# Optimization experiments

Measured on AMD Instinct MI355X. Metric: run time of the kernel, lower is better.

## Reference

```python
import jax, jax.numpy as jnp
import numpy as np

NS, NV = 48, 10
N_NODES, N_EDGES = 10000, 100000
N_EDGE_FEAT = 3 * NS  # 144
W_SS, W_VS, W_SV, W_VV = NS * NS, NV * NS, NS * NV, NV * NV
W_NUMEL = W_SS + W_VS + W_SV + W_VV  # 3364 = FullyConnectedTensorProduct.weight_numel
IN_DIM = NS + 3 * NV  # 78
EPS = 1e-5


def setup_inputs() -> dict:
    key = jax.random.key(0)
    ks = jax.random.split(key, 8)
    return {
        "node_attr": jax.random.normal(ks[0], (N_NODES, IN_DIM), jnp.float32),
        "edge_attr": jax.random.normal(ks[1], (N_EDGES, N_EDGE_FEAT), jnp.float32),
        "edge_sh": jax.random.normal(ks[2], (N_EDGES, 4), jnp.float32),
        "fc1_w": jax.random.normal(ks[3], (N_EDGE_FEAT, N_EDGE_FEAT), jnp.float32) / np.sqrt(N_EDGE_FEAT).astype(np.float32),
        "fc1_b": jnp.zeros((N_EDGE_FEAT,), jnp.float32),
        "fc2_w": jax.random.normal(ks[4], (N_EDGE_FEAT, W_NUMEL), jnp.float32) / np.sqrt(N_EDGE_FEAT).astype(np.float32),
        "fc2_b": jnp.zeros((W_NUMEL,), jnp.float32),
        "bn_weight": jnp.ones((NS + NV,), jnp.float32),
        "bn_bias": jnp.zeros((NS,), jnp.float32),
        "edge_index": jax.random.randint(ks[5], (2, N_EDGES), 0, N_NODES),
    }


def reference(node_attr, edge_attr, edge_sh, fc1_w, fc1_b, fc2_w, fc2_b, bn_weight, bn_bias, edge_index):
    edge_src, edge_dst = edge_index[0], edge_index[1]
    # --- gather node feats per edge, split into irreps ---
    x = node_attr[edge_dst]                      # [E, 78]
    xs = x[:, :NS]                               # [E, 48]  scalars (0e)
    xv = x[:, NS:].reshape(-1, NV, 3)            # [E, 10, 3] vectors (1o)
    s0 = edge_sh[:, 0]                           # [E]     sh 0e
    s1 = edge_sh[:, 1:4]                         # [E, 3]  sh 1o

    # --- per-edge TP weights from edge MLP ---
    w = jax.nn.relu(edge_attr @ fc1_w + fc1_b) @ fc2_w + fc2_b  # [E, 3364]
    w_ss = w[:, :W_SS].reshape(-1, NS, NS)
    w_vs = w[:, W_SS:W_SS + W_VS].reshape(-1, NV, NS)
    w_sv = w[:, W_SS + W_VS:W_SS + W_VS + W_SV].reshape(-1, NS, NV)
    w_vv = w[:, W_SS + W_VS + W_SV:].reshape(-1, NV, NV)

    # path normalization: 1/sqrt(mul_in * n_paths_into_output_irrep)
    a_ss = 1.0 / np.sqrt(NS * 2.0)
    a_vs = 1.0 / np.sqrt(NV * 2.0)
    a_sv = 1.0 / np.sqrt(NS * 2.0)
    a_vv = 1.0 / np.sqrt(NV * 2.0)

    # --- Clebsch-Gordan tensor product (fully connected, per-edge weights) ---
    # 0e (x) 0e -> 0e
    out_s = a_ss * jnp.einsum('ei,eio->eo', xs, w_ss) * s0[:, None]
    # 1o (x) 1o -> 0e  (CG = delta/sqrt(3))
    dot = jnp.einsum('eic,ec->ei', xv, s1) / np.sqrt(3.0)
    out_s = out_s + a_vs * jnp.einsum('ei,eio->eo', dot, w_vs)
    # 0e (x) 1o -> 1o
    out_v = a_sv * jnp.einsum('ei,eio->eo', xs, w_sv)[:, :, None] * s1[:, None, :]
    # 1o (x) 0e -> 1o
    out_v = out_v + a_vv * jnp.einsum('eic,eio->eoc', xv, w_vv) * s0[:, None, None]

    tp = jnp.concatenate([out_s, out_v.reshape(-1, 3 * NV)], axis=1)  # [E, 78]

    # --- scatter-mean to nodes ---
    sums = jax.ops.segment_sum(tp, edge_src, num_segments=N_NODES)
    cnt = jax.ops.segment_sum(jnp.ones((tp.shape[0],), tp.dtype), edge_src, num_segments=N_NODES)
    out = sums / jnp.maximum(cnt, 1.0)[:, None]

    # --- residual (in_dim == out_dim -> pad is a no-op) ---
    out = out + node_attr

    # --- equivariant batch norm (e3nn-style, batch statistics) ---
    os = out[:, :NS]
    ov = out[:, NS:].reshape(-1, NV, 3)
    mu = os.mean(0)
    var = os.var(0)
    os = (os - mu) / jnp.sqrt(var + EPS) * bn_weight[:NS] + bn_bias
    fn = (ov ** 2).sum(-1).mean(0) / 3.0  # component-normalized mean squared norm per channel
    ov = ov / jnp.sqrt(fn + EPS)[None, :, None] * bn_weight[NS:][None, :, None]
    return jnp.concatenate([os, ov.reshape(-1, 3 * NV)], axis=1)
```

## Files before the change

kernel.cpp:

```cpp
#include <hip/hip_runtime.h>
#include <hip/hip_bf16.h>

#define NS   48
#define NV   10
#define NEF  144
#define WN   3364
#define IND  78
#define NE   100000
#define NN   10000
#define EPS  1e-5f
#define HP   144
#define EB   128

#define A_SS 0.10206207261596575f
#define A_VS 0.22360679774997896f
#define A_SV 0.10206207261596575f
#define A_VV 0.22360679774997896f
#define RS3  0.5773502691896258f

typedef __attribute__((ext_vector_type(8)))  short    short8;
typedef __attribute__((ext_vector_type(16))) float    f32x16;
typedef __attribute__((ext_vector_type(4)))  int      int4v;
typedef __attribute__((ext_vector_type(4)))  float    float4v;
typedef __attribute__((ext_vector_type(2)))  __fp16   fp16x2;
typedef __attribute__((ext_vector_type(8)))  _Float16 half8;

#define MFMAH(a,b,c) __builtin_amdgcn_mfma_f32_32x32x16_f16((a),(b),(c),0,0,0)

#define TP_F    0
#define CNT_F   7800160
#define OFFS_F  7810160
#define CUR_F   7820164
#define EL_F    7830164
#define PART_F  7930164
#define RAW_F   8320164
#define WSBF_F  8320324

#define OFF_W1  0
#define OFF_B1  23040
#define OFF_B2  468480
#define OFF_B3  561664
#define N_PREP  608256

__device__ __forceinline__ short toh(float v) {
    return __builtin_bit_cast(short, (_Float16)v);
}
__device__ __forceinline__ float fromh(short s) {
    return (float)__builtin_bit_cast(_Float16, s);
}
__device__ __forceinline__ unsigned pkh2(float a, float b) {
    fp16x2 h = __builtin_amdgcn_cvt_pkrtz(a, b);
    return __builtin_bit_cast(unsigned, h);
}
__device__ __forceinline__ float waveReduceSum(float v) {
    #pragma unroll
    for (int o = 32; o > 0; o >>= 1) v += __shfl_down(v, o, 64);
    return v;
}
__device__ __forceinline__ void gl_lds16(const short* g, short* l) {
    __builtin_amdgcn_global_load_lds(
        (const __attribute__((address_space(1))) unsigned int*)g,
        (__attribute__((address_space(3))) unsigned int*)l, 16, 0, 0);
}

__device__ __forceinline__ float prep_fetch(int idx, const float* __restrict__ fc1_w,
                                            const float* __restrict__ fc2_w,
                                            const float* __restrict__ b2)
{
    float v = 0.f;
    if (idx < OFF_B1) {
        int r = idx;
        int tile = r / 4608, rem = r % 4608;
        int ks = rem / 512, l = (rem % 512) / 8, j = rem % 8;
        int n = tile * 32 + (l & 31);
        int k = ks * 16 + ((l >> 5) << 3) + j;
        v = (n < 144) ? fc1_w[k * 144 + n] : 0.f;
    } else if (idx < OFF_B2) {
        int r = idx - OFF_B1;
        if (r < 442368) {
            int i = r / 9216, rem = r % 9216;
            int tile = rem / 4608; rem %= 4608;
            int ks = rem / 512, l = (rem % 512) / 8, j = rem % 8;
            int n = tile * 32 + (l & 31);
            int k = ks * 16 + ((l >> 5) << 3) + j;
            if (n < 48)      v = fc2_w[(size_t)k * WN + i * 48 + n];
            else if (n < 58) v = fc2_w[(size_t)k * WN + 2784 + i * 10 + (n - 48)];
        } else {
            int rb = r - 442368;
            int tile = rb / 1536, rem = rb % 1536;
            int ks = rem / 512, l = (rem % 512) / 8, j = rem % 8;
            int n = tile * 32 + (l & 31);
            int k = ks * 16 + ((l >> 5) << 3) + j;
            if (n < 48)      v = b2[k * 48 + n];
            else if (n < 58) v = b2[2784 + k * 10 + (n - 48)];
        }
    } else if (idx < OFF_B3) {
        int r = idx - OFF_B2;
        if (r < 92160) {
            int i = r / 9216, rem = r % 9216;
            int tile = rem / 4608; rem %= 4608;
            int ks = rem / 512, l = (rem % 512) / 8, j = rem % 8;
            int n = tile * 32 + (l & 31);
            int k = ks * 16 + ((l >> 5) << 3) + j;
            if (n < 48) v = fc2_w[(size_t)k * WN + 2304 + i * 48 + n];
        } else {
            int rb = r - 92160;
            int tile = rb / 512, rem = rb % 512;
            int l = rem / 8, j = rem % 8;
            int n = tile * 32 + (l & 31);
            int k = ((l >> 5) << 3) + j;
            if (k < 10 && n < 48) v = b2[2304 + k * 48 + n];
        }
    } else {
        int r = idx - OFF_B3;
        if (r < 46080) {
            int i = r / 4608, rem = r % 4608;
            int ks = rem / 512, l = (rem % 512) / 8, j = rem % 8;
            int n = l & 31;
            int k = ks * 16 + ((l >> 5) << 3) + j;
            if (n < 10) v = fc2_w[(size_t)k * WN + 3264 + i * 10 + n];
        } else {
            int rb = r - 46080;
            int l = rb / 8, j = rb % 8;
            int n = l & 31;
            int k = ((l >> 5) << 3) + j;
            if (k < 10 && n < 10) v = b2[3264 + k * 10 + n];
        }
    }
    return v;
}

__global__ void prep_weights(const float* __restrict__ fc1_w,
                             const float* __restrict__ fc2_w,
                             const float* __restrict__ b2,
                             short* __restrict__ wsbf)
{
    int tid = blockIdx.x * 256 + threadIdx.x;
    if (tid >= N_PREP / 8) return;
    int base = tid * 8;
    short8 outv;
    #pragma unroll
    for (int j = 0; j < 8; ++j)
        outv[j] = toh(prep_fetch(base + j, fc1_w, fc2_w, b2));
    *reinterpret_cast<short8*>(wsbf + base) = outv;
}

__global__ void hist_kernel(const int* __restrict__ eidx, int* __restrict__ cntI)
{
    int e = blockIdx.x * 256 + threadIdx.x;
    if (e < NE) atomicAdd(&cntI[eidx[e]], 1);
}

__global__ __launch_bounds__(1024) void scan_kernel(const int* __restrict__ cntI,
                                                    int* __restrict__ offs,
                                                    int* __restrict__ cursor)
{
    __shared__ int part[1024];
    int t = threadIdx.x;
    int base = t * 10;
    int local[10];
    int s = 0;
    #pragma unroll
    for (int q = 0; q < 10; ++q) {
        int i = base + q;
        int v = (i < NN) ? cntI[i] : 0;
        local[q] = s; s += v;
    }
    part[t] = s;
    __syncthreads();
    for (int o = 1; o < 1024; o <<= 1) {
        int v = (t >= o) ? part[t - o] : 0;
        __syncthreads();
        part[t] += v;
        __syncthreads();
    }
    int prev = (t == 0) ? 0 : part[t - 1];
    #pragma unroll
    for (int q = 0; q < 10; ++q) {
        int i = base + q;
        if (i < NN) { int val = prev + local[q]; offs[i] = val; cursor[i] = val; }
    }
    if (t == 1023) offs[NN] = part[1023];
}

__global__ void scatter_kernel(const int* __restrict__ eidx,
                               int* __restrict__ cursor, int* __restrict__ elist)
{
    int e = blockIdx.x * 256 + threadIdx.x;
    if (e < NE) {
        int pos = atomicAdd(&cursor[eidx[e]], 1);
        elist[pos] = e;
    }
}

__global__ __launch_bounds__(256, 2) void fused_main(
    const float* __restrict__ node_attr, const float* __restrict__ edge_attr,
    const float* __restrict__ edge_sh,   const float* __restrict__ b1,
    const int*   __restrict__ eidx,      const short* __restrict__ wsbf,
    float* __restrict__ tp)
{
    __shared__ short ubuf[18432];
    __shared__ short xfT[96 * EB];
    __shared__ float pbuf[EB][10];
    __shared__ float s0s[EB];
    __shared__ float s1s[EB][3];

    const int t    = threadIdx.x;
    const int e0   = blockIdx.x * EB;
    const int lane = t & 63, wave = t >> 6;
    const int n32  = lane & 31, kh = lane >> 5;
    const int eL   = 32 * wave + n32;
    const int eLc  = min(e0 + eL, NE - 1);

    const short* W1L = wsbf + OFF_W1 + lane * 8;
    const short* B1L = wsbf + OFF_B1 + lane * 8;
    const short* B2L = wsbf + OFF_B2 + lane * 8;
    const short* B3L = wsbf + OFF_B3 + lane * 8;

    auto stageB = [&](const short* src, short* dst, int nfrag) {
        for (int f = wave; f < nfrag; f += 4)
            gl_lds16(src + f * 512 + lane * 8, dst + f * 512);
    };

    for (int idx = t; idx < 8 * EB; idx += 256) xfT[88 * EB + idx] = 0;

    if (t < EB) {
        int ee = e0 + t;
        if (ee < NE) {
            float4v sh = *reinterpret_cast<const float4v*>(edge_sh + (size_t)ee * 4);
            s0s[t] = sh.x; s1s[t][0] = sh.y; s1s[t][1] = sh.z; s1s[t][2] = sh.w;
        } else {
            s0s[t] = 0.f; s1s[t][0] = s1s[t][1] = s1s[t][2] = 0.f;
        }
    }

    {
        const int eg  = t & (EB - 1);
        const int jb  = t >> 7;
        const int egc = min(e0 + eg, NE - 1);
        const int dst = eidx[NE + egc];
        const float* na = node_attr + (size_t)dst * IND;
        for (int j = jb; j < IND; j += 2) {
            int slot = (j < NS) ? j : 58 + ((j - NS) % 3) * 10 + (j - NS) / 3;
            xfT[slot * EB + eg] = toh(na[j]);
        }
    }

    half8 afc[9];
    {
        const float* ea = edge_attr + (size_t)eLc * NEF + kh * 8;
        #pragma unroll
        for (int ks = 0; ks < 9; ++ks) {
            float4v lo = *reinterpret_cast<const float4v*>(ea + ks * 16);
            float4v hi = *reinterpret_cast<const float4v*>(ea + ks * 16 + 4);
            int4v v = { (int)pkh2(lo.x, lo.y), (int)pkh2(lo.z, lo.w),
                        (int)pkh2(hi.x, hi.y), (int)pkh2(hi.z, hi.w) };
            afc[ks] = __builtin_bit_cast(half8, v);
        }
    }
    __syncthreads();

    #pragma unroll
    for (int it = 0; it < 5; ++it) {
        int e = t & (EB - 1);
        int i = (t >> 7) + 2 * it;
        float d = fromh(xfT[(58 + i) * EB + e]) * s1s[e][0]
                + fromh(xfT[(68 + i) * EB + e]) * s1s[e][1]
                + fromh(xfT[(78 + i) * EB + e]) * s1s[e][2];
        xfT[(48 + i) * EB + e] = toh(d * RS3);
    }

    for (int pass = 0; pass < 3; ++pass) {
        int ntA = 2 * pass, ntB = 2 * pass + 1;
        bool hasB = (pass < 2);
        f32x16 accA = 0, accB = 0;
        #pragma unroll
        for (int ks = 0; ks < 9; ++ks) {
            half8 bA = *(const half8*)(W1L + (ntA * 9 + ks) * 512);
            accA = MFMAH(afc[ks], bA, accA);
            if (hasB) {
                half8 bB = *(const half8*)(W1L + (ntB * 9 + ks) * 512);
                accB = MFMAH(afc[ks], bB, accB);
            }
        }
        int colA = ntA * 32 + n32, colB = ntB * 32 + n32;
        float b1A = (colA < NEF) ? b1[colA] : 0.f;
        float b1B = (hasB && colB < NEF) ? b1[colB] : 0.f;
        #pragma unroll
        for (int r = 0; r < 16; ++r) {
            int row = (r & 3) + 8 * (r >> 2) + 4 * kh;
            int e = 32 * wave + row;
            if (colA < NEF) ubuf[e * HP + colA] = toh(fmaxf(accA[r] + b1A, 0.f));
            if (hasB)       ubuf[e * HP + colB] = toh(fmaxf(accB[r] + b1B, 0.f));
        }
    }

    half8 hh[9];
    #pragma unroll
    for (int ks = 0; ks < 9; ++ks)
        hh[ks] = *(const half8*)(ubuf + eL * HP + ks * 16 + kh * 8);
    __syncthreads();

    short* stg0 = ubuf;
    short* stg1 = ubuf + 9216;

    stageB(wsbf + OFF_B1, stg0, 18);
    __syncthreads();

    auto splat8 = [&](int slot) -> half8 {
        _Float16 xh = __builtin_bit_cast(_Float16, xfT[slot * EB + eL]);
        half8 r = { xh, xh, xh, xh, xh, xh, xh, xh };
        return r;
    };

    f32x16 acc1a = 0, acc1b = 0, acc2a = 0, acc2b = 0;
    {
        #pragma unroll 1
        for (int i = 0; i < 48; ++i) {
            short* cur = (i & 1) ? stg1 : stg0;
            short* nxt = (i & 1) ? stg0 : stg1;
            if (i < 47) stageB(wsbf + OFF_B1 + (i + 1) * 9216, nxt, 18);
            else        stageB(wsbf + OFF_B2, nxt, 18);
            half8 x8 = splat8(i);
            #pragma unroll
            for (int ks = 0; ks < 9; ++ks) {
                half8 a  = hh[ks] * x8;
                half8 b0 = *(const half8*)(cur + ks * 512 + lane * 8);
                half8 b1f= *(const half8*)(cur + 4608 + ks * 512 + lane * 8);
                acc1a = MFMAH(a, b0, acc1a);
                acc1b = MFMAH(a, b1f, acc1b);
            }
            __syncthreads();
        }
        #pragma unroll
        for (int ks = 0; ks < 3; ++ks) {
            short8 a;
            #pragma unroll
            for (int j = 0; j < 8; ++j)
                a[j] = xfT[(ks * 16 + kh * 8 + j) * EB + eL];
            half8 ah = __builtin_bit_cast(half8, a);
            half8 b0 = *(const half8*)(B1L + 442368 + ks * 512);
            half8 b1f= *(const half8*)(B1L + 442368 + 1536 + ks * 512);
            acc1a = MFMAH(ah, b0, acc1a);
            acc1b = MFMAH(ah, b1f, acc1b);
        }
    }
    {
        #pragma unroll 1
        for (int i = 0; i < 10; ++i) {
            short* cur = (i & 1) ? stg1 : stg0;
            short* nxt = (i & 1) ? stg0 : stg1;
            if (i < 9) stageB(wsbf + OFF_B2 + (i + 1) * 9216, nxt, 18);
            else       stageB(wsbf + OFF_B3, nxt, 9);
            half8 x8 = splat8(48 + i);
            #pragma unroll
            for (int ks = 0; ks < 9; ++ks) {
                half8 a  = hh[ks] * x8;
                half8 b0 = *(const half8*)(cur + ks * 512 + lane * 8);
                half8 b1f= *(const half8*)(cur + 4608 + ks * 512 + lane * 8);
                acc2a = MFMAH(a, b0, acc2a);
                acc2b = MFMAH(a, b1f, acc2b);
            }
            __syncthreads();
        }
        {
            short8 a;
            #pragma unroll
            for (int j = 0; j < 8; ++j)
                a[j] = xfT[(48 + kh * 8 + j) * EB + eL];
            half8 ah = __builtin_bit_cast(half8, a);
            half8 b0 = *(const half8*)(B2L + 92160);
            half8 b1f= *(const half8*)(B2L + 92160 + 512);
            acc2a = MFMAH(ah, b0, acc2a);
            acc2b = MFMAH(ah, b1f, acc2b);
        }
    }
    #pragma unroll
    for (int r = 0; r < 16; ++r) {
        int row = (r & 3) + 8 * (r >> 2) + 4 * kh;
        int e = 32 * wave + row;
        int ge = e0 + e;
        if (ge < NE) {
            float s0e = s0s[e];
            float* rowp = tp + (size_t)ge * IND;
            rowp[n32] = A_SS * s0e * acc1a[r] + A_VS * acc2a[r];
            int col = 32 + n32;
            if (col < 48) {
                rowp[col] = A_SS * s0e * acc1b[r] + A_VS * acc2b[r];
            } else if (col < 58) {
                pbuf[e][col - 48] = A_SV * acc1b[r];
            }
        }
    }
    {
        f32x16 acc30 = 0, acc31 = 0, acc32 = 0;
        #pragma unroll 1
        for (int i = 0; i < 10; ++i) {
            short* cur = (i & 1) ? stg1 : stg0;
            short* nxt = (i & 1) ? stg0 : stg1;
            if (i < 9) stageB(wsbf + OFF_B3 + (i + 1) * 4608, nxt, 9);
            half8 x0 = splat8(58 + i), x1 = splat8(68 + i), x2 = splat8(78 + i);
            #pragma unroll
            for (int ks = 0; ks < 9; ++ks) {
                half8 b0 = *(const half8*)(cur + ks * 512 + lane * 8);
                acc30 = MFMAH(hh[ks] * x0, b0, acc30);
                acc31 = MFMAH(hh[ks] * x1, b0, acc31);
                acc32 = MFMAH(hh[ks] * x2, b0, acc32);
            }
            __syncthreads();
        }
        {
            half8 bb = *(const half8*)(B3L + 46080);
            short8 a;
            #pragma unroll
            for (int j = 0; j < 8; ++j) a[j] = xfT[(58 + kh * 8 + j) * EB + eL];
            acc30 = MFMAH(__builtin_bit_cast(half8, a), bb, acc30);
            #pragma unroll
            for (int j = 0; j < 8; ++j) a[j] = xfT[(68 + kh * 8 + j) * EB + eL];
            acc31 = MFMAH(__builtin_bit_cast(half8, a), bb, acc31);
            #pragma unroll
            for (int j = 0; j < 8; ++j) a[j] = xfT[(78 + kh * 8 + j) * EB + eL];
            acc32 = MFMAH(__builtin_bit_cast(half8, a), bb, acc32);
        }
        if (n32 < 10) {
            #pragma unroll
            for (int r = 0; r < 16; ++r) {
                int row = (r & 3) + 8 * (r >> 2) + 4 * kh;
                int e = 32 * wave + row;
                int ge = e0 + e;
                if (ge < NE) {
                    float p  = pbuf[e][n32];
                    float qs = A_VV * s0s[e];
                    size_t base = (size_t)ge * IND + 48 + n32 * 3;
                    tp[base + 0] = p * s1s[e][0] + qs * acc30[r];
                    tp[base + 1] = p * s1s[e][1] + qs * acc31[r];
                    tp[base + 2] = p * s1s[e][2] + qs * acc32[r];
                }
            }
        }
    }
}

__global__ __launch_bounds__(256) void gather_kernel(const float* __restrict__ tp,
                                                     const int* __restrict__ offs,
                                                     const int* __restrict__ elist,
                                                     const float* __restrict__ node_attr,
                                                     float* __restrict__ out,
                                                     float* __restrict__ partial)
{
    __shared__ float sS[IND], sQ[IND];
    int t = threadIdx.x;
    if (t < IND) { sS[t] = 0.f; sQ[t] = 0.f; }
    __syncthreads();

    int node = blockIdx.x * 4 + (t >> 6);
    int lane = t & 63;
    int beg = offs[node], end = offs[node + 1];
    float a0 = 0.f, a1 = 0.f;
    for (int p = beg; p < end; ++p) {
        int e = elist[p];
        const float* row = tp + (size_t)e * IND;
        a0 += row[lane];
        if (lane < 14) a1 += row[64 + lane];
    }
    float c = fmaxf((float)(end - beg), 1.0f);
    size_t base = (size_t)node * IND;
    float v0 = a0 / c + node_attr[base + lane];
    out[base + lane] = v0;
    atomicAdd(&sS[lane], v0);
    atomicAdd(&sQ[lane], v0 * v0);
    if (lane < 14) {
        float v1 = a1 / c + node_attr[base + 64 + lane];
        out[base + 64 + lane] = v1;
        atomicAdd(&sS[64 + lane], v1);
        atomicAdd(&sQ[64 + lane], v1 * v1);
    }
    __syncthreads();
    if (t < IND)            partial[(size_t)blockIdx.x * 156 + t] = sS[t];
    else if (t < 2 * IND)   partial[(size_t)blockIdx.x * 156 + t] = sQ[t - IND];
}

__global__ __launch_bounds__(256) void reduce_kernel(const float* __restrict__ partial,
                                                     float* __restrict__ raw)
{
    int f = blockIdx.x;
    float s = 0.f;
    for (int b = threadIdx.x; b < 2500; b += 256)
        s += partial[(size_t)b * 156 + f];
    s = waveReduceSum(s);
    __shared__ float r[4];
    int w = threadIdx.x >> 6, lane = threadIdx.x & 63;
    if (lane == 0) r[w] = s;
    __syncthreads();
    if (threadIdx.x == 0) raw[f] = r[0] + r[1] + r[2] + r[3];
}

__global__ void normalize_kernel(const float* __restrict__ raw,
                                 const float* __restrict__ bnw,
                                 const float* __restrict__ bnb,
                                 float* __restrict__ out)
{
    int idx = blockIdx.x * 256 + threadIdx.x;
    if (idx >= NN * IND) return;
    int j = idx % IND;
    float x = out[idx];
    const float inv = 1.0f / (float)NN;
    if (j < NS) {
        float mu  = raw[j] * inv;
        float var = raw[IND + j] * inv - mu * mu;
        out[idx] = (x - mu) * rsqrtf(var + EPS) * bnw[j] + bnb[j];
    } else {
        int v = (j - NS) / 3;
        float fn = (raw[IND + NS + 3 * v] + raw[IND + NS + 3 * v + 1] +
                    raw[IND + NS + 3 * v + 2]) * (inv / 3.0f);
        out[idx] = x * bnw[NS + v] * rsqrtf(fn + EPS);
    }
}

extern "C" void kernel_launch(void* const* d_in, const int* in_sizes, int n_in,
                              void* d_out, int out_size, void* d_ws, size_t ws_size,
                              hipStream_t stream)
{
    (void)in_sizes; (void)n_in; (void)out_size; (void)ws_size;
    const float* node_attr = (const float*)d_in[0];
    const float* edge_attr = (const float*)d_in[1];
    const float* edge_sh   = (const float*)d_in[2];
    const float* fc1_w     = (const float*)d_in[3];
    const float* fc1_b     = (const float*)d_in[4];
    const float* fc2_w     = (const float*)d_in[5];
    const float* fc2_b     = (const float*)d_in[6];
    const float* bn_w      = (const float*)d_in[7];
    const float* bn_b      = (const float*)d_in[8];
    const int*   eidx      = (const int*)d_in[9];

    float* wsf   = (float*)d_ws;
    float* tp    = wsf + TP_F;
    int*   cntI  = (int*)(wsf + CNT_F);
    int*   offs  = (int*)(wsf + OFFS_F);
    int*   cur   = (int*)(wsf + CUR_F);
    int*   elist = (int*)(wsf + EL_F);
    float* part  = wsf + PART_F;
    float* raw   = wsf + RAW_F;
    short* wsbf  = (short*)(wsf + WSBF_F);
    float* out   = (float*)d_out;

    (void)hipMemsetAsync(cntI, 0, NN * sizeof(int), stream);
    prep_weights<<<(N_PREP / 8 + 255) / 256, 256, 0, stream>>>(fc1_w, fc2_w, fc2_b, wsbf);
    hist_kernel<<<(NE + 255) / 256, 256, 0, stream>>>(eidx, cntI);
    scan_kernel<<<1, 1024, 0, stream>>>(cntI, offs, cur);
    scatter_kernel<<<(NE + 255) / 256, 256, 0, stream>>>(eidx, cur, elist);
    fused_main<<<(NE + EB - 1) / EB, 256, 0, stream>>>(node_attr, edge_attr, edge_sh,
                                                       fc1_b, eidx, wsbf, tp);
    gather_kernel<<<NN / 4, 256, 0, stream>>>(tp, offs, elist, node_attr, out, part);
    reduce_kernel<<<156, 256, 0, stream>>>(part, raw);
    normalize_kernel<<<(NN * IND + 255) / 256, 256, 0, stream>>>(raw, bn_w, bn_b, out);
}
```

Baseline: 326.7 us.

## Store per-edge TP output in fp16, fuse histogram into scan, transpose partials

Per-edge tensor-product results are now written as fp16 instead of fp32 and converted back during the gather, halving the intermediate write and read traffic. The histogram and prefix scan are merged into a single-block kernel that counts in shared memory, which removes a memset and a kernel launch. The stat partials are stored feature-major so the reduce kernel reads contiguously. The fp16 intermediate reduces accuracy, and the single-block histogram serialises 100k atomic adds on one CU.

Measured after the change: 339.8 us. 4.0% more time.

```diff
diff --git a/kernel.cpp b/kernel.cpp
--- a/kernel.cpp
+++ b/kernel.cpp
@@ -28,7 +28,6 @@
 #define MFMAH(a,b,c) __builtin_amdgcn_mfma_f32_32x32x16_f16((a),(b),(c),0,0,0)
 
 #define TP_F    0
-#define CNT_F   7800160
 #define OFFS_F  7810160
 #define CUR_F   7820164
 #define EL_F    7830164
@@ -145,25 +144,24 @@
     *reinterpret_cast<short8*>(wsbf + base) = outv;
 }
 
-__global__ void hist_kernel(const int* __restrict__ eidx, int* __restrict__ cntI)
-{
-    int e = blockIdx.x * 256 + threadIdx.x;
-    if (e < NE) atomicAdd(&cntI[eidx[e]], 1);
-}
-
-__global__ __launch_bounds__(1024) void scan_kernel(const int* __restrict__ cntI,
-                                                    int* __restrict__ offs,
-                                                    int* __restrict__ cursor)
-{
+__global__ __launch_bounds__(1024) void histscan_kernel(const int* __restrict__ eidx,
+                                                        int* __restrict__ offs,
+                                                        int* __restrict__ cursor)
+{
+    __shared__ int cnt[NN];
     __shared__ int part[1024];
     int t = threadIdx.x;
+    for (int i = t; i < NN; i += 1024) cnt[i] = 0;
+    __syncthreads();
+    for (int e = t; e < NE; e += 1024) atomicAdd(&cnt[eidx[e]], 1);
+    __syncthreads();
     int base = t * 10;
     int local[10];
     int s = 0;
     #pragma unroll
     for (int q = 0; q < 10; ++q) {
         int i = base + q;
-        int v = (i < NN) ? cntI[i] : 0;
+        int v = (i < NN) ? cnt[i] : 0;
         local[q] = s; s += v;
     }
     part[t] = s;
@@ -197,7 +195,7 @@
     const float* __restrict__ node_attr, const float* __restrict__ edge_attr,
     const float* __restrict__ edge_sh,   const float* __restrict__ b1,
     const int*   __restrict__ eidx,      const short* __restrict__ wsbf,
-    float* __restrict__ tp)
+    short* __restrict__ tp)
 {
     __shared__ short ubuf[18432];
     __shared__ short xfT[96 * EB];
@@ -382,11 +380,11 @@
         int ge = e0 + e;
         if (ge < NE) {
             float s0e = s0s[e];
-            float* rowp = tp + (size_t)ge * IND;
-            rowp[n32] = A_SS * s0e * acc1a[r] + A_VS * acc2a[r];
+            short* rowp = tp + (size_t)ge * IND;
+            rowp[n32] = toh(A_SS * s0e * acc1a[r] + A_VS * acc2a[r]);
             int col = 32 + n32;
             if (col < 48) {
-                rowp[col] = A_SS * s0e * acc1b[r] + A_VS * acc2b[r];
+                rowp[col] = toh(A_SS * s0e * acc1b[r] + A_VS * acc2b[r]);
             } else if (col < 58) {
                 pbuf[e][col - 48] = A_SV * acc1b[r];
             }
@@ -432,16 +430,16 @@
                     float p  = pbuf[e][n32];
                     float qs = A_VV * s0s[e];
                     size_t base = (size_t)ge * IND + 48 + n32 * 3;
-                    tp[base + 0] = p * s1s[e][0] + qs * acc30[r];
-                    tp[base + 1] = p * s1s[e][1] + qs * acc31[r];
-                    tp[base + 2] = p * s1s[e][2] + qs * acc32[r];
+                    tp[base + 0] = toh(p * s1s[e][0] + qs * acc30[r]);
+                    tp[base + 1] = toh(p * s1s[e][1] + qs * acc31[r]);
+                    tp[base + 2] = toh(p * s1s[e][2] + qs * acc32[r]);
                 }
             }
         }
     }
 }
 
-__global__ __launch_bounds__(256) void gather_kernel(const float* __restrict__ tp,
+__global__ __launch_bounds__(256) void gather_kernel(const short* __restrict__ tp,
                                                      const int* __restrict__ offs,
                                                      const int* __restrict__ elist,
                                                      const float* __restrict__ node_attr,
@@ -459,9 +457,9 @@
     float a0 = 0.f, a1 = 0.f;
     for (int p = beg; p < end; ++p) {
         int e = elist[p];
-        const float* row = tp + (size_t)e * IND;
-        a0 += row[lane];
-        if (lane < 14) a1 += row[64 + lane];
+        const short* row = tp + (size_t)e * IND;
+        a0 += fromh(row[lane]);
+        if (lane < 14) a1 += fromh(row[64 + lane]);
     }
     float c = fmaxf((float)(end - beg), 1.0f);
     size_t base = (size_t)node * IND;
@@ -476,8 +474,8 @@
         atomicAdd(&sQ[64 + lane], v1 * v1);
     }
     __syncthreads();
-    if (t < IND)            partial[(size_t)blockIdx.x * 156 + t] = sS[t];
-    else if (t < 2 * IND)   partial[(size_t)blockIdx.x * 156 + t] = sQ[t - IND];
+    if (t < IND)            partial[(size_t)t * 2500 + blockIdx.x] = sS[t];
+    else if (t < 2 * IND)   partial[(size_t)(t - IND + IND) * 2500 + blockIdx.x] = sQ[t - IND];
 }
 
 __global__ __launch_bounds__(256) void reduce_kernel(const float* __restrict__ partial,
@@ -486,7 +484,7 @@
     int f = blockIdx.x;
     float s = 0.f;
     for (int b = threadIdx.x; b < 2500; b += 256)
-        s += partial[(size_t)b * 156 + f];
+        s += partial[(size_t)f * 2500 + b];
     s = waveReduceSum(s);
     __shared__ float r[4];
     int w = threadIdx.x >> 6, lane = threadIdx.x & 63;
@@ -534,8 +532,7 @@
     const int*   eidx      = (const int*)d_in[9];
 
     float* wsf   = (float*)d_ws;
-    float* tp    = wsf + TP_F;
-    int*   cntI  = (int*)(wsf + CNT_F);
+    short* tp    = (short*)(wsf + TP_F);
     int*   offs  = (int*)(wsf + OFFS_F);
     int*   cur   = (int*)(wsf + CUR_F);
     int*   elist = (int*)(wsf + EL_F);
@@ -544,10 +541,8 @@
     short* wsbf  = (short*)(wsf + WSBF_F);
     float* out   = (float*)d_out;
 
-    (void)hipMemsetAsync(cntI, 0, NN * sizeof(int), stream);
     prep_weights<<<(N_PREP / 8 + 255) / 256, 256, 0, stream>>>(fc1_w, fc2_w, fc2_b, wsbf);
-    hist_kernel<<<(NE + 255) / 256, 256, 0, stream>>>(eidx, cntI);
-    scan_kernel<<<1, 1024, 0, stream>>>(cntI, offs, cur);
+    histscan_kernel<<<1, 1024, 0, stream>>>(eidx, offs, cur);
     scatter_kernel<<<(NE + 255) / 256, 256, 0, stream>>>(eidx, cur, elist);
     fused_main<<<(NE + EB - 1) / EB, 256, 0, stream>>>(node_attr, edge_attr, edge_sh,
                                                        fc1_b, eidx, wsbf, tp);
```
